# Performance work log

Hardware: AMD Instinct MI355X
Metric: run time of the kernel (lower is better)

The kernel has to match this reference:

```python
import jax, jax.numpy as jnp
import numpy as np

EPS = 1e-5
MAX_NORM = 1.0 - 1e-5  # clamp for atanh / ball projection


def mob_add(u, v):
    # Mobius addition on each d_ball (last dim), c=1
    uv = jnp.sum(u * v, axis=-1, keepdims=True)
    uu = jnp.sum(u * u, axis=-1, keepdims=True)
    vv = jnp.sum(v * v, axis=-1, keepdims=True)
    num = (1.0 + 2.0 * uv + vv) * u + (1.0 - uu) * v
    den = 1.0 + 2.0 * uv + uu * vv
    return num / jnp.maximum(den, EPS)


def log_map_zero(y):
    # log map at origin, per ball (last dim)
    n = jnp.linalg.norm(y, axis=-1, keepdims=True)
    n_c = jnp.clip(n, EPS, MAX_NORM)
    return jnp.arctanh(n_c) * y / n_c


def mob_mat_mul_d(W, x, d):
    # W: (n_in, d, n_out, d); x: (B, n_in, d) -> (B, n_out, d)
    # Mobius matvec on the flattened product-ball representation.
    B = x.shape[0]
    x_f = x.reshape(B, -1)                      # (B, n_in*d)
    W_f = W.reshape(x_f.shape[-1], -1)          # (n_in*d, n_out*d)
    Mx = x_f @ W_f                              # (B, n_out*d)
    x_n = jnp.clip(jnp.linalg.norm(x_f, axis=-1, keepdims=True), EPS, MAX_NORM)
    Mx_n = jnp.maximum(jnp.linalg.norm(Mx, axis=-1, keepdims=True), EPS)
    res = jnp.tanh(Mx_n / x_n * jnp.arctanh(x_n)) * (Mx / Mx_n)
    return res.reshape(B, -1, d)


def mob_pointwise_prod(x, u):
    # diagonal Mobius scaling of hyperbolic x by euclidean gate u, per ball
    ux = u * x
    x_n = jnp.clip(jnp.linalg.norm(x, axis=-1, keepdims=True), EPS, MAX_NORM)
    ux_n = jnp.maximum(jnp.linalg.norm(ux, axis=-1, keepdims=True), EPS)
    return jnp.tanh(ux_n / x_n * jnp.arctanh(x_n)) * (ux / ux_n)


def transition(W, h, U, x, b, d):
    Wh = mob_mat_mul_d(W, h, d)
    Ux = mob_mat_mul_d(U, x, d)
    return mob_add(mob_add(Wh, Ux), b)


def setup_inputs() -> dict:
    key = jax.random.key(0)
    ks = jax.random.split(key, 8)
    B, I, H, D = 16384, 256, 256, 4
    k = (1.0 / H) ** 0.5
    # scale points to lie strictly inside the Poincare ball
    hyp_x = 0.02 * jax.random.normal(ks[0], (B, I, D), dtype=jnp.float32)
    hidden = 0.02 * jax.random.normal(ks[1], (B, H, D), dtype=jnp.float32)
    mk = lambda kk, n_in: jax.random.uniform(kk, (n_in, D, H, D), minval=-k, maxval=k, dtype=jnp.float32)
    return dict(
        hyp_x=hyp_x, hidden=hidden,
        w_z=mk(ks[2], H), w_r=mk(ks[3], H), w_h=mk(ks[4], H),
        u_z=mk(ks[5], I), u_r=mk(ks[6], I), u_h=mk(ks[7], I),
        b_z=jnp.zeros((H, D), jnp.float32),
        b_r=jnp.zeros((H, D), jnp.float32),
        b_h=jnp.zeros((H, D), jnp.float32),
    )


def reference(hyp_x, hidden, w_z, w_r, w_h, u_z, u_r, u_h, b_z, b_r, b_h):
    d = hyp_x.shape[-1]
    z = jax.nn.sigmoid(log_map_zero(transition(w_z, hidden, u_z, hyp_x, b_z, d)))
    r = jax.nn.sigmoid(log_map_zero(transition(w_r, hidden, u_r, hyp_x, b_r, d)))
    r_point_h = mob_pointwise_prod(hidden, r)
    # NOTE: original code uses u_r here (not u_h) -- kept faithful
    h_tilde = transition(w_h, r_point_h, u_r, hyp_x, b_h, d)
    minus_h_oplus_htilde = mob_add(-hidden, h_tilde)
    new_h = mob_add(hidden, mob_pointwise_prod(minus_h_oplus_htilde, z))
    return new_h
```

## Files before the change

### kernel.cpp

```cpp
#include <hip/hip_runtime.h>
#include <stdint.h>

#define EPSF 1e-5f
#define MAXNF (1.0f - 1e-5f)

typedef __attribute__((ext_vector_type(8))) short short8;
typedef __attribute__((ext_vector_type(4))) float floatx4;

__device__ __forceinline__ unsigned short f2bf(float f){
  union { float f; uint32_t u; } v; v.f = f;
  return (unsigned short)((v.u + 0x7FFFu + ((v.u >> 16) & 1u)) >> 16);
}
__device__ __forceinline__ float bf_lo(uint32_t u){
  union { uint32_t u; float f; } v; v.u = u << 16; return v.f;
}
__device__ __forceinline__ float bf_hi(uint32_t u){
  union { uint32_t u; float f; } v; v.u = u & 0xffff0000u; return v.f;
}
__device__ __forceinline__ uint32_t cvtpk(float lo, float hi){
  uint32_t r; asm("v_cvt_pk_bf16_f32 %0, %1, %2" : "=v"(r) : "v"(lo), "v"(hi));
  return r;
}
__device__ __forceinline__ float fsqrt(float x){ return __builtin_amdgcn_sqrtf(x); }

__device__ __forceinline__ float4 ld_ball(const unsigned short* rowp, int b){
  const uint2 u = *(const uint2*)(rowp + 4*b);
  return make_float4(bf_lo(u.x), bf_hi(u.x), bf_lo(u.y), bf_hi(u.y));
}
__device__ __forceinline__ void st_ball(unsigned short* rowp, int b, float4 f){
  uint2 u; u.x = cvtpk(f.x, f.y); u.y = cvtpk(f.z, f.w);
  *(uint2*)(rowp + 4*b) = u;
}

__device__ __forceinline__ void gload16(const void* g, void* l){
  __builtin_amdgcn_global_load_lds(
      (__attribute__((address_space(1))) void*)(uintptr_t)g,
      (__attribute__((address_space(3))) void*)l, 16, 0, 0);
}

__device__ __forceinline__ float fatanh(float x){
  return 0.5f * __logf(__fdividef(1.f + x, 1.f - x));
}
__device__ __forceinline__ float ftanh_pos(float x){
  const float t = __expf(-2.f * x);
  return __fdividef(1.f - t, 1.f + t);
}
__device__ __forceinline__ float fsig(float x){
  return __fdividef(1.f, 1.f + __expf(-x));
}

__device__ __forceinline__ float wsum(float v){
  #pragma unroll
  for (int o = 32; o; o >>= 1) v += __shfl_xor(v, o);
  return v;
}

__device__ __forceinline__ float dot4(const float4 a, const float4 b){
  return a.x*b.x + a.y*b.y + a.z*b.z + a.w*b.w;
}
__device__ __forceinline__ float4 scal4(const float4 a, float s){
  return make_float4(a.x*s, a.y*s, a.z*s, a.w*s);
}
__device__ __forceinline__ float clipn(float n){ return fminf(fmaxf(n, EPSF), MAXNF); }

__device__ __forceinline__ float4 mob_add4(const float4 u, const float4 v){
  const float uv = dot4(u,v), uu = dot4(u,u), vv = dot4(v,v);
  const float cu = 1.f + 2.f*uv + vv, cv = 1.f - uu;
  const float inv = __fdividef(1.f, fmaxf(1.f + 2.f*uv + uu*vv, EPSF));
  return make_float4((cu*u.x + cv*v.x)*inv, (cu*u.y + cv*v.y)*inv,
                     (cu*u.z + cv*v.z)*inv, (cu*u.w + cv*v.w)*inv);
}
__device__ __forceinline__ float4 logmap_sig4(const float4 y){
  const float nc = clipn(fsqrt(dot4(y,y)));
  const float s = __fdividef(fatanh(nc), nc);
  return make_float4(fsig(s*y.x), fsig(s*y.y), fsig(s*y.z), fsig(s*y.w));
}
__device__ __forceinline__ float4 mob_pp4(const float4 x, const float4 u){
  const float4 ux = make_float4(u.x*x.x, u.y*x.y, u.z*x.z, u.w*x.w);
  const float xn = clipn(fsqrt(dot4(x,x)));
  const float uxn = fmaxf(fsqrt(dot4(ux,ux)), EPSF);
  const float s = __fdividef(ftanh_pos(__fdividef(uxn, xn) * fatanh(xn)), uxn);
  return scal4(ux, s);
}

__global__ void cast_norm_k(const float* __restrict__ X, unsigned short* __restrict__ Xbf,
                            float* __restrict__ nrm){
  const int lane = threadIdx.x & 63;
  const int row  = blockIdx.x*4 + (threadIdx.x >> 6);
  const float4* xr = (const float4*)(X + (size_t)row*1024);
  unsigned short* br_ = Xbf + (size_t)row*1024;
  float ss = 0.f;
  #pragma unroll
  for (int i = 0; i < 4; ++i){
    const int b = lane + 64*i;
    const float4 v = xr[b];
    st_ball(br_, b, v);
    ss += dot4(v, v);
  }
  ss = wsum(ss);
  if (lane == 0) nrm[row] = fsqrt(ss);
}

__global__ void wcast_k(const float* __restrict__ W, unsigned short* __restrict__ Wt){
  __shared__ float tile[32][33];
  const int tx = threadIdx.x, ty = threadIdx.y;
  const int k0 = blockIdx.x * 32, n0 = blockIdx.y * 32;
  #pragma unroll
  for (int i = 0; i < 4; ++i)
    tile[ty + i*8][tx] = W[(size_t)(k0 + ty + i*8) * 1024 + n0 + tx];
  __syncthreads();
  #pragma unroll
  for (int i = 0; i < 4; ++i)
    Wt[(size_t)(n0 + ty + i*8) * 1024 + k0 + tx] = f2bf(tile[tx][ty + i*8]);
}

#define NT 16

#define BARFENCE do { __builtin_amdgcn_s_barrier(); asm volatile("" ::: "memory"); } while(0)
#define LDA4(dst, MO, BUF) do { _Pragma("unroll") for (int m_=0;m_<4;++m_) \
  _Pragma("unroll") for (int k_=0;k_<2;++k_) \
    dst[m_][k_] = *(const short8*)(smem + (BUF)*32768 + abase + (MO+m_)*2048 + ((((k_<<2)+kg)^x7)<<4)); } while(0)
#define LDB2(dst, NO, BUF) do { _Pragma("unroll") for (int n_=0;n_<2;++n_) \
  _Pragma("unroll") for (int k_=0;k_<2;++k_) \
    dst[n_][k_] = *(const short8*)(smem + (BUF)*32768 + bbase + (NO+n_)*2048 + ((((k_<<2)+kg)^x7)<<4)); } while(0)
#define QUAD(AF, MO, BF, NO) do { _Pragma("unroll") for (int m_=0;m_<4;++m_) \
  _Pragma("unroll") for (int n_=0;n_<2;++n_) \
  _Pragma("unroll") for (int k_=0;k_<2;++k_) \
    acc[MO+m_][NO+n_] = __builtin_amdgcn_mfma_f32_16x16x32_bf16(AF[m_][k_], BF[n_][k_], acc[MO+m_][NO+n_], 0,0,0); } while(0)

__global__ __launch_bounds__(512, 2) void gemm8_k(const unsigned short* __restrict__ A,
                                                  const unsigned short* __restrict__ Bt,
                                                  unsigned short* __restrict__ C,
                                                  int lda, int ldc, int lnx){
  __shared__ unsigned char smem[131072];
  const int tid = threadIdx.x;
  const int lane = tid & 63, w = tid >> 6;
  const int wm = w >> 2, wn = w & 3;
  const int lr = lane & 15, kg = lane >> 4;
  const int x7 = lr & 7;

  const int wg  = blockIdx.x;
  const int xcd = wg & 7, q = wg >> 3;
  const int bx  = q & ((1 << lnx) - 1);
  const int by  = (xcd << 3) + (q >> lnx);
  const int row0 = by * 256, col0 = bx * 256;

  const int abase = (wm*128 + lr)*128;
  const int bbase = 65536 + (wn*64 + lr)*128;

  floatx4 acc[8][4] = {};

  auto stageH = [&](int regionByte, const unsigned short* src, int srow0, int ld, int kt){
    #pragma unroll
    for (int call = 0; call < 2; ++call){
      const int L  = (call << 9) + tid;
      const int rl = L >> 3;
      const int cc = (L & 7) ^ (rl & 7);
      gload16(src + (size_t)(srow0 + rl)*ld + kt*64 + cc*8,
              smem + regionByte + L*16);
    }
  };
  auto stageA = [&](int kt, int h){ stageH((kt&1)*32768 + h*16384, A, row0 + h*128, lda, kt); };
  auto stageB = [&](int kt, int h){ stageH(65536 + (kt&1)*32768 + h*16384, Bt, col0 + h*128, 1024, kt); };

  stageA(0,0); stageA(0,1); stageB(0,0); stageB(0,1);
  stageA(1,0); stageA(1,1); stageB(1,0); stageB(1,1);
  asm volatile("s_waitcnt vmcnt(8)" ::: "memory");
  BARFENCE;

  short8 aL[4][2], aH[4][2], bA[2][2], bB[2][2];
  LDA4(aL, 0, 0);
  LDB2(bA, 0, 0);

  for (int t = 0; t < NT; ++t){
    const int bufb = t & 1;
    LDB2(bB, 2, bufb);
    BARFENCE;
    __builtin_amdgcn_s_setprio(1); QUAD(aL, 0, bA, 0); __builtin_amdgcn_s_setprio(0);
    BARFENCE;
    LDA4(aH, 4, bufb);
    BARFENCE;
    __builtin_amdgcn_s_setprio(1); QUAD(aL, 0, bB, 2); __builtin_amdgcn_s_setprio(0);
    BARFENCE;
    if (t+2 < NT){
      stageB(t+2,0); stageB(t+2,1);
      asm volatile("s_waitcnt vmcnt(4)" ::: "memory");
    } else if (t+1 < NT){
      asm volatile("s_waitcnt vmcnt(0)" ::: "memory");
    }
    BARFENCE;
    __builtin_amdgcn_s_setprio(1); QUAD(aH, 4, bB, 2); __builtin_amdgcn_s_setprio(0);
    if (t+1 < NT) LDA4(aL, 0, bufb^1);
    BARFENCE;
    if (t+2 < NT){ stageA(t+2,0); stageA(t+2,1); }
    BARFENCE;
    __builtin_amdgcn_s_setprio(1); QUAD(aH, 4, bA, 0); __builtin_amdgcn_s_setprio(0);
    if (t+1 < NT) LDB2(bA, 0, bufb^1);
    BARFENCE;
  }

  const int crow = row0 + wm*128;
  const int ccol = col0 + wn*64 + lr;
  #pragma unroll
  for (int m = 0; m < 8; ++m){
    #pragma unroll
    for (int j = 0; j < 4; ++j){
      unsigned short* cp = C + (size_t)(crow + m*16 + kg*4 + j)*ldc + ccol;
      #pragma unroll
      for (int n = 0; n < 4; ++n) cp[n*16] = f2bf(acc[m][n][j]);
    }
  }
}

__global__ __launch_bounds__(256) __attribute__((amdgpu_waves_per_eu(4,4)))
void epi1_k(unsigned short* C1, unsigned short* C2, const unsigned short* hbf,
            const float* bz, const float* br,
            const float* h_nrm, const float* x_nrm, float* rph_nrm){
  const int lane = threadIdx.x & 63;
  const int row  = blockIdx.x*4 + (threadIdx.x >> 6);
  unsigned short* c1lo = C1 + (size_t)row*2048;
  unsigned short* c1hi = c1lo + 1024;
  unsigned short* c2lo = C2 + (size_t)row*2048;
  unsigned short* c2hi = c2lo + 1024;
  const unsigned short* hr = hbf + (size_t)row*1024;

  float4 mzh[4], mrh[4], mzx[4], mrx[4];
  float s0 = 0.f, s1 = 0.f, s2 = 0.f, s3 = 0.f;
  #pragma unroll
  for (int i = 0; i < 4; ++i){
    const int b = lane + 64*i;
    mzh[i] = ld_ball(c1lo, b); mrh[i] = ld_ball(c1hi, b);
    mzx[i] = ld_ball(c2lo, b); mrx[i] = ld_ball(c2hi, b);
    s0 += dot4(mzh[i], mzh[i]); s1 += dot4(mzx[i], mzx[i]);
    s2 += dot4(mrh[i], mrh[i]); s3 += dot4(mrx[i], mrx[i]);
  }
  s0 = wsum(s0); s1 = wsum(s1); s2 = wsum(s2); s3 = wsum(s3);

  const float nMzh = fmaxf(fsqrt(s0), EPSF);
  const float nMzx = fmaxf(fsqrt(s1), EPSF);
  const float nMrh = fmaxf(fsqrt(s2), EPSF);
  const float nMrx = fmaxf(fsqrt(s3), EPSF);
  const float hnc = clipn(h_nrm[row]), xnc = clipn(x_nrm[row]);
  const float atH = fatanh(hnc), atX = fatanh(xnc);
  const float swz = __fdividef(ftanh_pos(__fdividef(nMzh, hnc)*atH), nMzh);
  const float suz = __fdividef(ftanh_pos(__fdividef(nMzx, xnc)*atX), nMzx);
  const float swr = __fdividef(ftanh_pos(__fdividef(nMrh, hnc)*atH), nMrh);
  const float sur = __fdividef(ftanh_pos(__fdividef(nMrx, xnc)*atX), nMrx);

  float sr = 0.f;
  #pragma unroll
  for (int i = 0; i < 4; ++i){
    const int b = lane + 64*i;
    const float4 bz4 = ((const float4*)bz)[b];
    const float4 br4 = ((const float4*)br)[b];
    const float4 z4  = logmap_sig4(mob_add4(mob_add4(scal4(mzh[i],swz), scal4(mzx[i],suz)), bz4));
    const float4 UxR = scal4(mrx[i], sur);
    const float4 r4  = logmap_sig4(mob_add4(mob_add4(scal4(mrh[i],swr), UxR), br4));
    st_ball(c1lo, b, z4);
    st_ball(c1hi, b, UxR);
    const float4 h4  = ld_ball(hr, b);
    const float4 rph = mob_pp4(h4, r4);
    st_ball(c2lo, b, rph);
    sr += dot4(rph, rph);
  }
  sr = wsum(sr);
  if (lane == 0) rph_nrm[row] = fsqrt(sr);
}

__global__ __launch_bounds__(256) __attribute__((amdgpu_waves_per_eu(4,4)))
void epi2_k(const unsigned short* C1, const unsigned short* C2,
            const unsigned short* hbf, const float* bh,
            const float* rph_nrm, float* out){
  const int lane = threadIdx.x & 63;
  const int row  = blockIdx.x*4 + (threadIdx.x >> 6);
  const unsigned short* c1lo = C1 + (size_t)row*2048;
  const unsigned short* c1hi = c1lo + 1024;
  const unsigned short* c2hi = C2 + (size_t)row*2048 + 1024;
  const unsigned short* hr = hbf + (size_t)row*1024;
  float4* outr = (float4*)(out + (size_t)row*1024);

  float4 mh[4];
  float ss = 0.f;
  #pragma unroll
  for (int i = 0; i < 4; ++i){
    mh[i] = ld_ball(c2hi, lane + 64*i);
    ss += dot4(mh[i], mh[i]);
  }
  ss = wsum(ss);
  const float nMh = fmaxf(fsqrt(ss), EPSF);
  const float rnc = clipn(rph_nrm[row]);
  const float swh = __fdividef(ftanh_pos(__fdividef(nMh, rnc)*fatanh(rnc)), nMh);

  #pragma unroll
  for (int i = 0; i < 4; ++i){
    const int b = lane + 64*i;
    const float4 WhH = scal4(mh[i], swh);
    const float4 Ux4 = ld_ball(c1hi, b);
    const float4 bh4 = ((const float4*)bh)[b];
    const float4 ht  = mob_add4(mob_add4(WhH, Ux4), bh4);
    const float4 h4  = ld_ball(hr, b);
    const float4 nh4 = make_float4(-h4.x, -h4.y, -h4.z, -h4.w);
    const float4 m4  = mob_add4(nh4, ht);
    const float4 z4  = ld_ball(c1lo, b);
    const float4 p4  = mob_pp4(m4, z4);
    outr[b] = mob_add4(h4, p4);
  }
}

extern "C" void kernel_launch(void* const* d_in, const int* in_sizes, int n_in,
                              void* d_out, int out_size, void* d_ws, size_t ws_size,
                              hipStream_t stream) {
  (void)in_sizes; (void)n_in; (void)out_size; (void)ws_size;
  const float* hyp_x  = (const float*)d_in[0];
  const float* hidden = (const float*)d_in[1];
  const float* w_z = (const float*)d_in[2];
  const float* w_r = (const float*)d_in[3];
  const float* w_h = (const float*)d_in[4];
  const float* u_z = (const float*)d_in[5];
  const float* u_r = (const float*)d_in[6];
  const float* b_z = (const float*)d_in[8];
  const float* b_r = (const float*)d_in[9];
  const float* b_h = (const float*)d_in[10];
  float* out = (float*)d_out;

  const size_t NROW = 16384, MAT = NROW*1024;
  unsigned short* hbf = (unsigned short*)d_ws;
  unsigned short* xbf = hbf + MAT;
  unsigned short* C1  = xbf + MAT;
  unsigned short* wzr = C1 + 2*MAT;
  unsigned short* uzr = wzr + 2*1048576;
  unsigned short* wht = uzr + 2*1048576;
  float* h_n   = (float*)(wht + 1048576);
  float* x_n   = h_n + NROW;
  float* rph_n = x_n + NROW;
  unsigned short* C2 = (unsigned short*)d_out;

  cast_norm_k<<<dim3(4096), dim3(256), 0, stream>>>(hidden, hbf, h_n);
  cast_norm_k<<<dim3(4096), dim3(256), 0, stream>>>(hyp_x, xbf, x_n);

  dim3 wg(32, 32), wb(32, 8);
  wcast_k<<<wg, wb, 0, stream>>>(w_z, wzr);
  wcast_k<<<wg, wb, 0, stream>>>(w_r, wzr + 1048576);
  wcast_k<<<wg, wb, 0, stream>>>(u_z, uzr);
  wcast_k<<<wg, wb, 0, stream>>>(u_r, uzr + 1048576);
  wcast_k<<<wg, wb, 0, stream>>>(w_h, wht);

  gemm8_k<<<dim3(512), dim3(512), 0, stream>>>(hbf, wzr, C1, 1024, 2048, 3);
  gemm8_k<<<dim3(512), dim3(512), 0, stream>>>(xbf, uzr, C2, 1024, 2048, 3);

  epi1_k<<<dim3(4096), dim3(256), 0, stream>>>(C1, C2, hbf, b_z, b_r, h_n, x_n, rph_n);

  gemm8_k<<<dim3(256), dim3(512), 0, stream>>>(C2, wht, C2 + 1024, 2048, 2048, 2);

  epi2_k<<<dim3(4096), dim3(256), 0, stream>>>(C1, C2, hbf, b_h, rph_n, out);
}
```

Baseline: 324.0 us.

## Merge cast launches, swizzle row-block order, reuse xbf for rph

```diff
diff --git a/kernel.cpp b/kernel.cpp
--- a/kernel.cpp
+++ b/kernel.cpp
@@ -83,12 +83,20 @@
   return scal4(ux, s);
 }
 
-__global__ void cast_norm_k(const float* __restrict__ X, unsigned short* __restrict__ Xbf,
-                            float* __restrict__ nrm){
+__device__ __forceinline__ int rowswz(int b){ return ((b & 7) << 9) + (b >> 3); }
+
+__global__ void cast2_k(const float* __restrict__ H, const float* __restrict__ X,
+                        unsigned short* __restrict__ Hbf, unsigned short* __restrict__ Xbf,
+                        float* __restrict__ h_n, float* __restrict__ x_n){
+  int blk = blockIdx.x;
+  const float* src; unsigned short* dst; float* nrm;
+  if (blk < 4096){ src = H; dst = Hbf; nrm = h_n; }
+  else { src = X; dst = Xbf; nrm = x_n; blk -= 4096; }
+  blk = rowswz(blk);
   const int lane = threadIdx.x & 63;
-  const int row  = blockIdx.x*4 + (threadIdx.x >> 6);
-  const float4* xr = (const float4*)(X + (size_t)row*1024);
-  unsigned short* br_ = Xbf + (size_t)row*1024;
+  const int row  = blk*4 + (threadIdx.x >> 6);
+  const float4* xr = (const float4*)(src + (size_t)row*1024);
+  unsigned short* br_ = dst + (size_t)row*1024;
   float ss = 0.f;
   #pragma unroll
   for (int i = 0; i < 4; ++i){
@@ -101,7 +109,20 @@
   if (lane == 0) nrm[row] = fsqrt(ss);
 }
 
-__global__ void wcast_k(const float* __restrict__ W, unsigned short* __restrict__ Wt){
+__global__ void wcast5_k(const float* __restrict__ w_z, const float* __restrict__ w_r,
+                         const float* __restrict__ u_z, const float* __restrict__ u_r,
+                         const float* __restrict__ w_h,
+                         unsigned short* __restrict__ wzr, unsigned short* __restrict__ uzr,
+                         unsigned short* __restrict__ wht){
+  const int m = blockIdx.z;
+  const float* W; unsigned short* Wt;
+  switch (m){
+    case 0: W = w_z; Wt = wzr;           break;
+    case 1: W = w_r; Wt = wzr + 1048576; break;
+    case 2: W = u_z; Wt = uzr;           break;
+    case 3: W = u_r; Wt = uzr + 1048576; break;
+    default: W = w_h; Wt = wht;          break;
+  }
   __shared__ float tile[32][33];
   const int tx = threadIdx.x, ty = threadIdx.y;
   const int k0 = blockIdx.x * 32, n0 = blockIdx.y * 32;
@@ -213,16 +234,17 @@
 }
 
 __global__ __launch_bounds__(256) __attribute__((amdgpu_waves_per_eu(4,4)))
-void epi1_k(unsigned short* C1, unsigned short* C2, const unsigned short* hbf,
-            const float* bz, const float* br,
+void epi1_k(unsigned short* C1, const unsigned short* C2, const unsigned short* hbf,
+            unsigned short* rphb, const float* bz, const float* br,
             const float* h_nrm, const float* x_nrm, float* rph_nrm){
   const int lane = threadIdx.x & 63;
-  const int row  = blockIdx.x*4 + (threadIdx.x >> 6);
+  const int row  = rowswz(blockIdx.x)*4 + (threadIdx.x >> 6);
   unsigned short* c1lo = C1 + (size_t)row*2048;
   unsigned short* c1hi = c1lo + 1024;
-  unsigned short* c2lo = C2 + (size_t)row*2048;
-  unsigned short* c2hi = c2lo + 1024;
+  const unsigned short* c2lo = C2 + (size_t)row*2048;
+  const unsigned short* c2hi = c2lo + 1024;
   const unsigned short* hr = hbf + (size_t)row*1024;
+  unsigned short* rr = rphb + (size_t)row*1024;
 
   float4 mzh[4], mrh[4], mzx[4], mrx[4];
   float s0 = 0.f, s1 = 0.f, s2 = 0.f, s3 = 0.f;
@@ -260,7 +282,7 @@
     st_ball(c1hi, b, UxR);
     const float4 h4  = ld_ball(hr, b);
     const float4 rph = mob_pp4(h4, r4);
-    st_ball(c2lo, b, rph);
+    st_ball(rr, b, rph);
     sr += dot4(rph, rph);
   }
   sr = wsum(sr);
@@ -272,7 +294,7 @@
             const unsigned short* hbf, const float* bh,
             const float* rph_nrm, float* out){
   const int lane = threadIdx.x & 63;
-  const int row  = blockIdx.x*4 + (threadIdx.x >> 6);
+  const int row  = rowswz(blockIdx.x)*4 + (threadIdx.x >> 6);
   const unsigned short* c1lo = C1 + (size_t)row*2048;
   const unsigned short* c1hi = c1lo + 1024;
   const unsigned short* c2hi = C2 + (size_t)row*2048 + 1024;
@@ -335,22 +357,17 @@
   float* rph_n = x_n + NROW;
   unsigned short* C2 = (unsigned short*)d_out;
 
-  cast_norm_k<<<dim3(4096), dim3(256), 0, stream>>>(hidden, hbf, h_n);
-  cast_norm_k<<<dim3(4096), dim3(256), 0, stream>>>(hyp_x, xbf, x_n);
-
-  dim3 wg(32, 32), wb(32, 8);
-  wcast_k<<<wg, wb, 0, stream>>>(w_z, wzr);
-  wcast_k<<<wg, wb, 0, stream>>>(w_r, wzr + 1048576);
-  wcast_k<<<wg, wb, 0, stream>>>(u_z, uzr);
-  wcast_k<<<wg, wb, 0, stream>>>(u_r, uzr + 1048576);
-  wcast_k<<<wg, wb, 0, stream>>>(w_h, wht);
+  cast2_k<<<dim3(8192), dim3(256), 0, stream>>>(hidden, hyp_x, hbf, xbf, h_n, x_n);
+  wcast5_k<<<dim3(32,32,5), dim3(32,8), 0, stream>>>(w_z, w_r, u_z, u_r, w_h,
+                                                     wzr, uzr, wht);
 
   gemm8_k<<<dim3(512), dim3(512), 0, stream>>>(hbf, wzr, C1, 1024, 2048, 3);
   gemm8_k<<<dim3(512), dim3(512), 0, stream>>>(xbf, uzr, C2, 1024, 2048, 3);
 
-  epi1_k<<<dim3(4096), dim3(256), 0, stream>>>(C1, C2, hbf, b_z, b_r, h_n, x_n, rph_n);
-
-  gemm8_k<<<dim3(256), dim3(512), 0, stream>>>(C2, wht, C2 + 1024, 2048, 2048, 2);
+  epi1_k<<<dim3(4096), dim3(256), 0, stream>>>(C1, C2, hbf, xbf ,
+                                               b_z, b_r, h_n, x_n, rph_n);
+
+  gemm8_k<<<dim3(256), dim3(512), 0, stream>>>(xbf, wht, C2 + 1024, 1024, 2048, 2);
 
   epi2_k<<<dim3(4096), dim3(256), 0, stream>>>(C1, C2, hbf, b_h, rph_n, out);
 }
```

New measurement: 316.9 us. 2.2% less time.
